# Optimization experiments

Measured on AMD Instinct MI355X. Metric: run time of the kernel, lower is better.

## Reference

```python
import jax, jax.numpy as jnp
import numpy as np

# Emformer config (from torchaudio.models.Emformer in BasicNet4)
D, H, FFN, L = 512, 4, 128, 4      # input_dim, num_heads, ffn_dim, num_layers
SEG, RC = 4, 1                     # segment_length, right_context_length
B, T = 8, 1025
U = T - RC                         # utterance length = 1024
NSEG = -(-U // SEG)                # 256 segments
R = NSEG * RC                      # total right-context frames = 256
DH = D // H


def _right_context_indices():
    # torchaudio _gen_right_context: segment i's right context = frames [(i+1)*SEG : (i+1)*SEG+RC],
    # last block = input[T-RC:]
    idx = [np.arange((i + 1) * SEG, (i + 1) * SEG + RC) for i in range(NSEG - 1)]
    idx.append(np.arange(T - RC, T))
    return np.concatenate(idx)


def _attention_mask():
    # Rows / cols ordered [right-context blocks (seg order), utterance frames].
    # A query belonging to segment i may attend to segment i's right-context block
    # and segment i's utterance frames (left_context_length=0, no memory bank).
    seg_rc = np.repeat(np.arange(NSEG), RC)
    seg_u = np.arange(U) // SEG
    seg_q = np.concatenate([seg_rc, seg_u])
    seg_k = np.concatenate([seg_rc, seg_u])
    return seg_q[:, None] == seg_k[None, :]  # (R+U, R+U), True = allowed


def _ln(x, g, b, eps=1e-5):
    mu = jnp.mean(x, -1, keepdims=True)
    var = jnp.mean(jnp.square(x - mu), -1, keepdims=True)
    return (x - mu) * jax.lax.rsqrt(var + eps) * g + b


def setup_inputs() -> dict:
    key = jax.random.key(0)
    ks = jax.random.split(key, 8)
    s = 0.02
    return {
        "x": jax.random.normal(ks[0], (B, T, D), jnp.float32),
        "Wq": jax.random.normal(ks[1], (L, D, D), jnp.float32) * s,
        "bq": jnp.zeros((L, D), jnp.float32),
        "Wkv": jax.random.normal(ks[2], (L, 2 * D, D), jnp.float32) * s,
        "bkv": jnp.zeros((L, 2 * D), jnp.float32),
        "Wo": jax.random.normal(ks[3], (L, D, D), jnp.float32) * s,
        "bo": jnp.zeros((L, D), jnp.float32),
        "W1": jax.random.normal(ks[4], (L, FFN, D), jnp.float32) * s,
        "b1": jnp.zeros((L, FFN), jnp.float32),
        "W2": jax.random.normal(ks[5], (L, D, FFN), jnp.float32) * s,
        "b2": jnp.zeros((L, D), jnp.float32),
        "ln_in_g": jnp.ones((L, D), jnp.float32),
        "ln_in_b": jnp.zeros((L, D), jnp.float32),
        "ff_ln_g": jnp.ones((L, D), jnp.float32),
        "ff_ln_b": jnp.zeros((L, D), jnp.float32),
        "ln_out_g": jnp.ones((L, D), jnp.float32),
        "ln_out_b": jnp.zeros((L, D), jnp.float32),
    }


def reference(x, Wq, bq, Wkv, bkv, Wo, bo, W1, b1, W2, b2,
              ln_in_g, ln_in_b, ff_ln_g, ff_ln_b, ln_out_g, ln_out_b):
    rc_idx = jnp.asarray(_right_context_indices())
    allowed = jnp.asarray(_attention_mask())
    scale = DH ** -0.5
    u = x[:, :U]          # (B, U, D) utterance
    r = x[:, rc_idx]      # (B, R, D) gathered right-context blocks
    for l in range(L):
        cat = jnp.concatenate([r, u], axis=1)            # (B, R+U, D)
        ln = _ln(cat, ln_in_g[l], ln_in_b[l])            # pre-attention LN
        q = (ln @ Wq[l].T + bq[l]).reshape(B, R + U, H, DH)
        kv = ln @ Wkv[l].T + bkv[l]
        k = kv[..., :D].reshape(B, R + U, H, DH)
        v = kv[..., D:].reshape(B, R + U, H, DH)
        scores = jnp.einsum("bqhd,bkhd->bhqk", q * scale, k)
        scores = jnp.where(allowed, scores, -jnp.inf)
        probs = jax.nn.softmax(scores, axis=-1)
        attn = jnp.einsum("bhqk,bkhd->bqhd", probs, v).reshape(B, R + U, D)
        rc_out = attn @ Wo[l].T + bo[l] + cat            # residual w/ pre-LN input
        h = _ln(rc_out, ff_ln_g[l], ff_ln_b[l])
        h = jax.nn.relu(h @ W1[l].T + b1[l]) @ W2[l].T + b2[l]
        rc_out = _ln(rc_out + h, ln_out_g[l], ln_out_b[l])
        r, u = rc_out[:, :R], rc_out[:, R:]
    return u.mean(axis=1)  # (B, D): mean-pool over utterance frames
```

## Files before the change

kernel.cpp:

```cpp
#include <hip/hip_runtime.h>
#include <cstdint>
#include <cstddef>

#define D_    512
#define H_    4
#define DH_   128
#define FFN_  128
#define L_    4
#define B_    8
#define T_    1025
#define U_    1024
#define NSEG_ 256
#define R_    256
#define TOT_  1280
#define M_    (B_*TOT_)
#define CH_   1536

typedef __attribute__((ext_vector_type(8))) short bf16x8;
typedef __attribute__((ext_vector_type(4))) float f32x4;
typedef unsigned short u16;

__device__ __forceinline__ u16 f2bf(float f) {
  unsigned u = __builtin_bit_cast(unsigned, f);
  u += 0x7fff + ((u >> 16) & 1);
  return (u16)(u >> 16);
}
__device__ __forceinline__ float bf2f(u16 h) {
  unsigned u = ((unsigned)h) << 16;
  return __builtin_bit_cast(float, u);
}

__device__ __forceinline__ void gload_lds16(const void* g, void* l) {
  __builtin_amdgcn_global_load_lds(
      (const __attribute__((address_space(1))) unsigned*)g,
      (__attribute__((address_space(3))) unsigned*)l, 16, 0, 0);
}

__global__ __launch_bounds__(256)
void cvt_all_k(const float* __restrict__ Wq, const float* __restrict__ Wkv,
               const float* __restrict__ Wo, const float* __restrict__ W1,
               const float* __restrict__ W2, const float* __restrict__ bq,
               const float* __restrict__ bkv,
               u16* __restrict__ WQKVb, u16* __restrict__ Wob,
               u16* __restrict__ W1b, u16* __restrict__ W2b,
               float* __restrict__ bQKV) {
  int i4 = blockIdx.x * 256 + threadIdx.x;
  if (i4 < 786432) {
    int e = i4 * 4;
    int l = e / 786432;
    int rem = e - l * 786432;
    int n = rem >> 9, k = rem & 511;
    const float* src = (n < 512) ? (Wq + (size_t)l * 262144 + n * 512 + k)
                                 : (Wkv + (size_t)l * 524288 + (n - 512) * 512 + k);
    float4 v = *(const float4*)src;
    ushort4 o; o.x = f2bf(v.x); o.y = f2bf(v.y); o.z = f2bf(v.z); o.w = f2bf(v.w);
    *(ushort4*)(WQKVb + e) = o;
  } else if (i4 < 1048576) {
    int e = (i4 - 786432) * 4;
    float4 v = *(const float4*)(Wo + e);
    ushort4 o; o.x = f2bf(v.x); o.y = f2bf(v.y); o.z = f2bf(v.z); o.w = f2bf(v.w);
    *(ushort4*)(Wob + e) = o;
  } else if (i4 < 1114112) {
    int e = (i4 - 1048576) * 4;
    float4 v = *(const float4*)(W1 + e);
    ushort4 o; o.x = f2bf(v.x); o.y = f2bf(v.y); o.z = f2bf(v.z); o.w = f2bf(v.w);
    *(ushort4*)(W1b + e) = o;
  } else if (i4 < 1179648) {
    int e = (i4 - 1114112) * 4;
    float4 v = *(const float4*)(W2 + e);
    ushort4 o; o.x = f2bf(v.x); o.y = f2bf(v.y); o.z = f2bf(v.z); o.w = f2bf(v.w);
    *(ushort4*)(W2b + e) = o;
  } else if (i4 < 1181184) {
    int e = (i4 - 1179648) * 4;
    int l = e / 1536, n = e - l * 1536;
#pragma unroll
    for (int t = 0; t < 4; ++t) {
      int nn = n + t;
      bQKV[e + t] = (nn < 512) ? bq[l * 512 + nn] : bkv[l * 1024 + (nn - 512)];
    }
  }
}

__global__ __launch_bounds__(256)
void gather_ln_k(const float* __restrict__ x, const float* __restrict__ g,
                 const float* __restrict__ bb, float* __restrict__ X,
                 u16* __restrict__ LNb) {
  int row = blockIdx.x;
  int tid = threadIdx.x;
  int b = row / TOT_, p = row % TOT_;
  int t = (p < R_) ? ((p < R_ - 1) ? 4 * (p + 1) : (T_ - 1)) : (p - R_);
  const float* xr = x + ((size_t)b * T_ + t) * D_;
  float e0 = xr[tid], e1 = xr[tid + 256];
  X[(size_t)row * D_ + tid] = e0;
  X[(size_t)row * D_ + tid + 256] = e1;
  float s = e0 + e1, ss = e0 * e0 + e1 * e1;
#pragma unroll
  for (int off = 32; off > 0; off >>= 1) {
    s  += __shfl_down(s, off);
    ss += __shfl_down(ss, off);
  }
  __shared__ float red[10];
  int wid = tid >> 6, lane = tid & 63;
  if (lane == 0) { red[wid] = s; red[4 + wid] = ss; }
  __syncthreads();
  if (tid == 0) {
    float S = red[0] + red[1] + red[2] + red[3];
    float SS = red[4] + red[5] + red[6] + red[7];
    float mu = S * (1.0f / D_);
    float var = SS * (1.0f / D_) - mu * mu;
    if (var < 0.f) var = 0.f;
    red[8] = mu; red[9] = rsqrtf(var + 1e-5f);
  }
  __syncthreads();
  float mu = red[8], rs = red[9];
  u16* yr = LNb + (size_t)row * D_;
  yr[tid]       = f2bf((e0 - mu) * rs * g[tid]       + bb[tid]);
  yr[tid + 256] = f2bf((e1 - mu) * rs * g[tid + 256] + bb[tid + 256]);
}

#define GBM 128
#define GBN 128
#define GBK 32

__global__ __launch_bounds__(256)
void gemm_qkv(const u16* __restrict__ A, const u16* __restrict__ Bw,
              const float* __restrict__ bias, u16* __restrict__ Cout,
              int M, int N, int K) {
  __shared__ __align__(16) u16 As[GBM * GBK];
  __shared__ __align__(16) u16 Bs[GBN * GBK];
  const int tid = threadIdx.x;
  const int wid = tid >> 6;
  const int lane = tid & 63;
  const int bm = blockIdx.y * GBM;
  const int bn = blockIdx.x * GBN;
  const int wr = wid >> 1, wc = wid & 1;

  const int srow = tid >> 2;
  const int skoff = (tid & 3) << 3;

  f32x4 acc[4][4] = {};

  const u16* Ag0 = A  + (size_t)(bm + srow)      * K + skoff;
  const u16* Ag1 = A  + (size_t)(bm + 64 + srow) * K + skoff;
  const u16* Bg0 = Bw + (size_t)(bn + srow)      * K + skoff;
  const u16* Bg1 = Bw + (size_t)(bn + 64 + srow) * K + skoff;
  u16* AsW0 = &As[(size_t)(wid * 16)      * GBK];
  u16* AsW1 = &As[(size_t)(64 + wid * 16) * GBK];
  u16* BsW0 = &Bs[(size_t)(wid * 16)      * GBK];
  u16* BsW1 = &Bs[(size_t)(64 + wid * 16) * GBK];

  const int lrow = lane & 15;
  const int lko  = (lane >> 4) * 16;

  for (int k0 = 0; k0 < K; k0 += GBK) {
    __syncthreads();
    gload_lds16(Ag0 + k0, AsW0);
    gload_lds16(Ag1 + k0, AsW1);
    gload_lds16(Bg0 + k0, BsW0);
    gload_lds16(Bg1 + k0, BsW1);
    __syncthreads();

    bf16x8 afrag[4], bfrag[4];
#pragma unroll
    for (int m = 0; m < 4; ++m) {
      int row = wr * 64 + m * 16 + lrow;
      afrag[m] = *(const bf16x8*)((const char*)As + row * (GBK * 2) + lko);
    }
#pragma unroll
    for (int n = 0; n < 4; ++n) {
      int col = wc * 64 + n * 16 + lrow;
      bfrag[n] = *(const bf16x8*)((const char*)Bs + col * (GBK * 2) + lko);
    }
#pragma unroll
    for (int m = 0; m < 4; ++m)
#pragma unroll
      for (int n = 0; n < 4; ++n)
        acc[m][n] = __builtin_amdgcn_mfma_f32_16x16x32_bf16(
            afrag[m], bfrag[n], acc[m][n], 0, 0, 0);
  }

  const int lcol  = lane & 15;
  const int lrow4 = (lane >> 4) * 4;
#pragma unroll
  for (int m = 0; m < 4; ++m) {
    int rowbase = bm + wr * 64 + m * 16 + lrow4;
#pragma unroll
    for (int n = 0; n < 4; ++n) {
      int col = bn + wc * 64 + n * 16 + lcol;
      float bv = bias[col];
#pragma unroll
      for (int j = 0; j < 4; ++j) {
        int row = rowbase + j;
        ((u16*)Cout)[(size_t)row * N + col] = f2bf(acc[m][n][j] + bv);
      }
    }
  }
}

template <int MODE>
__global__ __launch_bounds__(256)
void gemm_row_ln(const u16* __restrict__ A, const u16* __restrict__ Bw,
                 const float* __restrict__ bias, const float* __restrict__ Rsd,
                 float* __restrict__ Xout,
                 const float* __restrict__ g1, const float* __restrict__ b1,
                 const float* __restrict__ g2, const float* __restrict__ b2,
                 u16* __restrict__ OutBf, int K) {
  __shared__ __align__(16) u16 As[32 * 32];
  __shared__ __align__(16) u16 Bs[512 * 32];
  __shared__ float wsum[4][32], wss[4][32], mu_s[32], rs_s[32];
  const int tid = threadIdx.x;
  const int wid = tid >> 6, lane = tid & 63;
  const int bm = blockIdx.x * 32;
  const int l4 = lane >> 2;
  const int k8 = (lane & 3) << 3;
  const int lrow = lane & 15;
  const int lko  = (lane >> 4) * 16;

  f32x4 acc[2][8] = {};

  const u16* Ag = A + (size_t)(bm + (wid & 1) * 16 + l4) * K + k8;

  for (int k0 = 0; k0 < K; k0 += 32) {
    __syncthreads();
    if (wid < 2)
      gload_lds16(Ag + k0, (char*)As + (wid * 16) * 64);
#pragma unroll
    for (int p = 0; p < 8; ++p) {
      int row = wid * 128 + p * 16 + l4;
      gload_lds16(Bw + (size_t)row * K + k0 + k8,
                  (char*)Bs + (wid * 128 + p * 16) * 64);
    }
    __syncthreads();

    bf16x8 af[2], bf[8];
#pragma unroll
    for (int m = 0; m < 2; ++m)
      af[m] = *(const bf16x8*)((const char*)As + (m * 16 + lrow) * 64 + lko);
#pragma unroll
    for (int n = 0; n < 8; ++n)
      bf[n] = *(const bf16x8*)((const char*)Bs + (wid * 128 + n * 16 + lrow) * 64 + lko);
#pragma unroll
    for (int m = 0; m < 2; ++m)
#pragma unroll
      for (int n = 0; n < 8; ++n)
        acc[m][n] = __builtin_amdgcn_mfma_f32_16x16x32_bf16(
            af[m], bf[n], acc[m][n], 0, 0, 0);
  }

  const int lcol = lane & 15;
  const int lr4 = (lane >> 4) * 4;
#pragma unroll
  for (int n = 0; n < 8; ++n) {
    int col = wid * 128 + n * 16 + lcol;
    float bv = bias[col];
#pragma unroll
    for (int m = 0; m < 2; ++m)
#pragma unroll
      for (int j = 0; j < 4; ++j) {
        int row = bm + m * 16 + lr4 + j;
        float t = acc[m][n][j] + bv + Rsd[(size_t)row * D_ + col];
        if (MODE == 0) Xout[(size_t)row * D_ + col] = t;
        acc[m][n][j] = t;
      }
  }

  {
    float s0[2][4] = {}, s1[2][4] = {};
#pragma unroll
    for (int m = 0; m < 2; ++m)
#pragma unroll
      for (int n = 0; n < 8; ++n)
#pragma unroll
        for (int j = 0; j < 4; ++j) {
          float v = acc[m][n][j];
          s0[m][j] += v; s1[m][j] += v * v;
        }
#pragma unroll
    for (int off = 1; off < 16; off <<= 1)
#pragma unroll
      for (int m = 0; m < 2; ++m)
#pragma unroll
        for (int j = 0; j < 4; ++j) {
          s0[m][j] += __shfl_xor(s0[m][j], off);
          s1[m][j] += __shfl_xor(s1[m][j], off);
        }
    if ((lane & 15) == 0) {
#pragma unroll
      for (int m = 0; m < 2; ++m)
#pragma unroll
        for (int j = 0; j < 4; ++j) {
          int r = m * 16 + lr4 + j;
          wsum[wid][r] = s0[m][j]; wss[wid][r] = s1[m][j];
        }
    }
  }
  __syncthreads();
  if (tid < 32) {
    float S  = wsum[0][tid] + wsum[1][tid] + wsum[2][tid] + wsum[3][tid];
    float SS = wss[0][tid] + wss[1][tid] + wss[2][tid] + wss[3][tid];
    float mu = S * (1.0f / D_);
    float var = SS * (1.0f / D_) - mu * mu;
    if (var < 0.f) var = 0.f;
    mu_s[tid] = mu; rs_s[tid] = rsqrtf(var + 1e-5f);
  }
  __syncthreads();

  float gg[8], bv2[8];
#pragma unroll
  for (int n = 0; n < 8; ++n) {
    int col = wid * 128 + n * 16 + lcol;
    gg[n] = g1[col]; bv2[n] = b1[col];
  }
#pragma unroll
  for (int m = 0; m < 2; ++m)
#pragma unroll
    for (int n = 0; n < 8; ++n) {
      int col = wid * 128 + n * 16 + lcol;
#pragma unroll
      for (int j = 0; j < 4; ++j) {
        int r = m * 16 + lr4 + j;
        int row = bm + r;
        float ln = (acc[m][n][j] - mu_s[r]) * rs_s[r] * gg[n] + bv2[n];
        if (MODE == 0) {
          OutBf[(size_t)row * D_ + col] = f2bf(ln);
        } else {
          Xout[(size_t)row * D_ + col] = ln;
          acc[m][n][j] = ln;
        }
      }
    }

  if (MODE == 1) {
    __syncthreads();
    {
      float s0[2][4] = {}, s1[2][4] = {};
#pragma unroll
      for (int m = 0; m < 2; ++m)
#pragma unroll
        for (int n = 0; n < 8; ++n)
#pragma unroll
          for (int j = 0; j < 4; ++j) {
            float v = acc[m][n][j];
            s0[m][j] += v; s1[m][j] += v * v;
          }
#pragma unroll
      for (int off = 1; off < 16; off <<= 1)
#pragma unroll
        for (int m = 0; m < 2; ++m)
#pragma unroll
          for (int j = 0; j < 4; ++j) {
            s0[m][j] += __shfl_xor(s0[m][j], off);
            s1[m][j] += __shfl_xor(s1[m][j], off);
          }
      if ((lane & 15) == 0) {
#pragma unroll
        for (int m = 0; m < 2; ++m)
#pragma unroll
          for (int j = 0; j < 4; ++j) {
            int r = m * 16 + lr4 + j;
            wsum[wid][r] = s0[m][j]; wss[wid][r] = s1[m][j];
          }
      }
    }
    __syncthreads();
    if (tid < 32) {
      float S  = wsum[0][tid] + wsum[1][tid] + wsum[2][tid] + wsum[3][tid];
      float SS = wss[0][tid] + wss[1][tid] + wss[2][tid] + wss[3][tid];
      float mu = S * (1.0f / D_);
      float var = SS * (1.0f / D_) - mu * mu;
      if (var < 0.f) var = 0.f;
      mu_s[tid] = mu; rs_s[tid] = rsqrtf(var + 1e-5f);
    }
    __syncthreads();
#pragma unroll
    for (int n = 0; n < 8; ++n) {
      int col = wid * 128 + n * 16 + lcol;
      gg[n] = g2[col]; bv2[n] = b2[col];
    }
#pragma unroll
    for (int m = 0; m < 2; ++m)
#pragma unroll
      for (int n = 0; n < 8; ++n) {
        int col = wid * 128 + n * 16 + lcol;
#pragma unroll
        for (int j = 0; j < 4; ++j) {
          int r = m * 16 + lr4 + j;
          int row = bm + r;
          float ln = (acc[m][n][j] - mu_s[r]) * rs_s[r] * gg[n] + bv2[n];
          OutBf[(size_t)row * D_ + col] = f2bf(ln);
        }
      }
  }
}

__global__ __launch_bounds__(256)
void gemm_ffn1(const u16* __restrict__ A, const u16* __restrict__ Bw,
               const float* __restrict__ bias, u16* __restrict__ Hout) {
  __shared__ __align__(16) u16 As[32 * 32];
  __shared__ __align__(16) u16 Bs[128 * 32];
  const int tid = threadIdx.x;
  const int wid = tid >> 6, lane = tid & 63;
  const int bm = blockIdx.x * 32;
  const int l4 = lane >> 2;
  const int k8 = (lane & 3) << 3;
  const int lrow = lane & 15;
  const int lko  = (lane >> 4) * 16;

  f32x4 acc[2][2] = {};
  const u16* Ag = A + (size_t)(bm + (wid & 1) * 16 + l4) * D_ + k8;

  for (int k0 = 0; k0 < D_; k0 += 32) {
    __syncthreads();
    if (wid < 2)
      gload_lds16(Ag + k0, (char*)As + (wid * 16) * 64);
#pragma unroll
    for (int p = 0; p < 2; ++p) {
      int row = wid * 32 + p * 16 + l4;
      gload_lds16(Bw + (size_t)row * D_ + k0 + k8,
                  (char*)Bs + (wid * 32 + p * 16) * 64);
    }
    __syncthreads();
    bf16x8 af[2], bf[2];
#pragma unroll
    for (int m = 0; m < 2; ++m)
      af[m] = *(const bf16x8*)((const char*)As + (m * 16 + lrow) * 64 + lko);
#pragma unroll
    for (int n = 0; n < 2; ++n)
      bf[n] = *(const bf16x8*)((const char*)Bs + (wid * 32 + n * 16 + lrow) * 64 + lko);
#pragma unroll
    for (int m = 0; m < 2; ++m)
#pragma unroll
      for (int n = 0; n < 2; ++n)
        acc[m][n] = __builtin_amdgcn_mfma_f32_16x16x32_bf16(
            af[m], bf[n], acc[m][n], 0, 0, 0);
  }

  const int lcol = lane & 15;
  const int lr4 = (lane >> 4) * 4;
#pragma unroll
  for (int m = 0; m < 2; ++m)
#pragma unroll
    for (int n = 0; n < 2; ++n) {
      int col = wid * 32 + n * 16 + lcol;
      float bv = bias[col];
#pragma unroll
      for (int j = 0; j < 4; ++j) {
        int row = bm + m * 16 + lr4 + j;
        float v = fmaxf(acc[m][n][j] + bv, 0.f);
        Hout[(size_t)row * FFN_ + col] = f2bf(v);
      }
    }
}

#define QLD 516
__global__ __launch_bounds__(256)
void attn_k(const u16* __restrict__ QKV, u16* __restrict__ O) {
  int bs = blockIdx.x;
  int b = bs >> 8, s = bs & 255;
  __shared__ float Qs[5][QLD];
  __shared__ float Ks[5][QLD];
  __shared__ float Vs[5][QLD];
  __shared__ float P[H_][5][5];
  int tid = threadIdx.x;
  const float scale = 0.08838834764831845f;
  int rows[5];
  rows[0] = s;
#pragma unroll
  for (int i = 1; i < 5; ++i) rows[i] = R_ + 4 * s + (i - 1);
  for (int idx = tid; idx < 5 * D_; idx += 256) {
    int i = idx >> 9, c = idx & (D_ - 1);
    size_t base = ((size_t)b * TOT_ + rows[i]) * CH_;
    Qs[i][c] = bf2f(QKV[base + c]) * scale;
    Ks[i][c] = bf2f(QKV[base + D_ + c]);
    Vs[i][c] = bf2f(QKV[base + 2 * D_ + c]);
  }
  __syncthreads();
  int h = tid >> 6, lane = tid & 63;
  if (lane < 25) {
    int i = lane / 5, j = lane % 5;
    float sum = 0.f;
    const float* qp = &Qs[i][h * DH_];
    const float* kp = &Ks[j][h * DH_];
#pragma unroll 8
    for (int d = 0; d < DH_; ++d) sum += qp[d] * kp[d];
    P[h][i][j] = sum;
  }
  __syncthreads();
  if (lane < 5) {
    int i = lane;
    float m = P[h][i][0];
#pragma unroll
    for (int j = 1; j < 5; ++j) m = fmaxf(m, P[h][i][j]);
    float e[5], ssum = 0.f;
#pragma unroll
    for (int j = 0; j < 5; ++j) { e[j] = __expf(P[h][i][j] - m); ssum += e[j]; }
    float inv = 1.0f / ssum;
#pragma unroll
    for (int j = 0; j < 5; ++j) P[h][i][j] = e[j] * inv;
  }
  __syncthreads();
  for (int idx = lane; idx < 5 * DH_; idx += 64) {
    int i = idx >> 7, d = idx & (DH_ - 1);
    float o = 0.f;
#pragma unroll
    for (int j = 0; j < 5; ++j) o += P[h][i][j] * Vs[j][h * DH_ + d];
    O[((size_t)b * TOT_ + rows[i]) * D_ + h * DH_ + d] = f2bf(o);
  }
}

__global__ __launch_bounds__(256)
void mean_part_k(const float* __restrict__ X, float* __restrict__ part) {
  int d = blockIdx.x * 256 + threadIdx.x;
  int jc = blockIdx.y;
  int b = blockIdx.z;
  float acc = 0.f;
  const float* base = X + ((size_t)b * TOT_ + R_ + jc * 128) * D_ + d;
  for (int j = 0; j < 128; ++j) acc += base[(size_t)j * D_];
  part[((size_t)b * 8 + jc) * D_ + d] = acc;
}

__global__ __launch_bounds__(256)
void mean_final_k(const float* __restrict__ part, float* __restrict__ out) {
  int i = blockIdx.x * 256 + threadIdx.x;
  int b = i >> 9, d = i & (D_ - 1);
  float acc = 0.f;
#pragma unroll
  for (int c = 0; c < 8; ++c) acc += part[((size_t)b * 8 + c) * D_ + d];
  out[i] = acc * (1.0f / U_);
}

extern "C" void kernel_launch(void* const* d_in, const int* in_sizes, int n_in,
                              void* d_out, int out_size, void* d_ws, size_t ws_size,
                              hipStream_t stream) {
  const float* x      = (const float*)d_in[0];
  const float* Wq     = (const float*)d_in[1];
  const float* bq     = (const float*)d_in[2];
  const float* Wkv    = (const float*)d_in[3];
  const float* bkv    = (const float*)d_in[4];
  const float* Wo     = (const float*)d_in[5];
  const float* bo     = (const float*)d_in[6];
  const float* W1     = (const float*)d_in[7];
  const float* b1     = (const float*)d_in[8];
  const float* W2     = (const float*)d_in[9];
  const float* b2     = (const float*)d_in[10];
  const float* ln_in_g  = (const float*)d_in[11];
  const float* ln_in_b  = (const float*)d_in[12];
  const float* ff_ln_g  = (const float*)d_in[13];
  const float* ff_ln_b  = (const float*)d_in[14];
  const float* ln_out_g = (const float*)d_in[15];
  const float* ln_out_b = (const float*)d_in[16];
  float* out = (float*)d_out;

  char* wsb = (char*)d_ws;
  float* X     = (float*)wsb;
  u16*   LNbuf = (u16*)(wsb + 20971520);
  u16*   QKV   = (u16*)(wsb + 31457280);
  u16*   ATT   = (u16*)(wsb + 62914560);
  u16*   LN2b  = (u16*)(wsb + 73400320);
  u16*   Hb    = (u16*)(wsb + 83886080);
  float* part  = (float*)(wsb + 86507520);
  u16*   WQKVb = (u16*)(wsb + 86638592);
  u16*   Wob   = (u16*)(wsb + 92930048);
  u16*   W1b   = (u16*)(wsb + 95027200);
  u16*   W2b   = (u16*)(wsb + 95551488);
  float* bQKV  = (float*)(wsb + 96075776);

  cvt_all_k<<<4614, 256, 0, stream>>>(Wq, Wkv, Wo, W1, W2, bq, bkv,
                                      WQKVb, Wob, W1b, W2b, bQKV);
  gather_ln_k<<<M_, 256, 0, stream>>>(x, ln_in_g, ln_in_b, X, LNbuf);

  for (int l = 0; l < L_; ++l) {
    const u16* WQKV_l = WQKVb + (size_t)l * CH_ * D_;
    const u16* Wo_l   = Wob   + (size_t)l * D_ * D_;
    const u16* W1_l   = W1b   + (size_t)l * FFN_ * D_;
    const u16* W2_l   = W2b   + (size_t)l * D_ * FFN_;
    const float* bQKV_l = bQKV + (size_t)l * CH_;
    const float* bo_l = bo + (size_t)l * D_;
    const float* b1_l = b1 + (size_t)l * FFN_;
    const float* b2_l = b2 + (size_t)l * D_;

    gemm_qkv<<<dim3(CH_ / GBN, M_ / GBM), 256, 0, stream>>>(
        LNbuf, WQKV_l, bQKV_l, QKV, M_, CH_, D_);

    attn_k<<<B_ * NSEG_, 256, 0, stream>>>(QKV, ATT);

    gemm_row_ln<0><<<M_ / 32, 256, 0, stream>>>(
        ATT, Wo_l, bo_l, X, X,
        ff_ln_g + l * D_, ff_ln_b + l * D_, nullptr, nullptr, LN2b, D_);

    gemm_ffn1<<<M_ / 32, 256, 0, stream>>>(LN2b, W1_l, b1_l, Hb);

    if (l < L_ - 1) {
      gemm_row_ln<1><<<M_ / 32, 256, 0, stream>>>(
          Hb, W2_l, b2_l, X, X,
          ln_out_g + l * D_, ln_out_b + l * D_,
          ln_in_g + (l + 1) * D_, ln_in_b + (l + 1) * D_, LNbuf, FFN_);
    } else {
      gemm_row_ln<2><<<M_ / 32, 256, 0, stream>>>(
          Hb, W2_l, b2_l, X, X,
          ln_out_g + l * D_, ln_out_b + l * D_,
          nullptr, nullptr, nullptr, FFN_);
    }
  }

  mean_part_k<<<dim3(2, 8, 8), 256, 0, stream>>>(X, part);
  mean_final_k<<<(B_ * D_) / 256, 256, 0, stream>>>(part, out);
}
```

Baseline: 437.7 us.

## Halve row tiles in LN GEMMs, swizzle QKV grid per XCD, vectorize attention loads

```diff
diff --git a/kernel.cpp b/kernel.cpp
--- a/kernel.cpp
+++ b/kernel.cpp
@@ -118,21 +118,23 @@
   yr[tid + 256] = f2bf((e1 - mu) * rs * g[tid + 256] + bb[tid + 256]);
 }
 
-#define GBM 128
-#define GBN 128
 #define GBK 32
 
 __global__ __launch_bounds__(256)
 void gemm_qkv(const u16* __restrict__ A, const u16* __restrict__ Bw,
-              const float* __restrict__ bias, u16* __restrict__ Cout,
-              int M, int N, int K) {
-  __shared__ __align__(16) u16 As[GBM * GBK];
-  __shared__ __align__(16) u16 Bs[GBN * GBK];
+              const float* __restrict__ bias, u16* __restrict__ Cout) {
+  __shared__ __align__(16) u16 As[128 * GBK];
+  __shared__ __align__(16) u16 Bs[128 * GBK];
   const int tid = threadIdx.x;
   const int wid = tid >> 6;
   const int lane = tid & 63;
-  const int bm = blockIdx.y * GBM;
-  const int bn = blockIdx.x * GBN;
+  const int bid = blockIdx.x;
+  const int xcd = bid & 7;
+  const int t = bid >> 3;
+  const int cb = t % 12;
+  const int rb = xcd * 10 + t / 12;
+  const int bm = rb * 128;
+  const int bn = cb * 128;
   const int wr = wid >> 1, wc = wid & 1;
 
   const int srow = tid >> 2;
@@ -140,10 +142,10 @@
 
   f32x4 acc[4][4] = {};
 
-  const u16* Ag0 = A  + (size_t)(bm + srow)      * K + skoff;
-  const u16* Ag1 = A  + (size_t)(bm + 64 + srow) * K + skoff;
-  const u16* Bg0 = Bw + (size_t)(bn + srow)      * K + skoff;
-  const u16* Bg1 = Bw + (size_t)(bn + 64 + srow) * K + skoff;
+  const u16* Ag0 = A  + (size_t)(bm + srow)      * D_ + skoff;
+  const u16* Ag1 = A  + (size_t)(bm + 64 + srow) * D_ + skoff;
+  const u16* Bg0 = Bw + (size_t)(bn + srow)      * D_ + skoff;
+  const u16* Bg1 = Bw + (size_t)(bn + 64 + srow) * D_ + skoff;
   u16* AsW0 = &As[(size_t)(wid * 16)      * GBK];
   u16* AsW1 = &As[(size_t)(64 + wid * 16) * GBK];
   u16* BsW0 = &Bs[(size_t)(wid * 16)      * GBK];
@@ -152,7 +154,7 @@
   const int lrow = lane & 15;
   const int lko  = (lane >> 4) * 16;
 
-  for (int k0 = 0; k0 < K; k0 += GBK) {
+  for (int k0 = 0; k0 < D_; k0 += GBK) {
     __syncthreads();
     gload_lds16(Ag0 + k0, AsW0);
     gload_lds16(Ag1 + k0, AsW1);
@@ -191,7 +193,7 @@
 #pragma unroll
       for (int j = 0; j < 4; ++j) {
         int row = rowbase + j;
-        ((u16*)Cout)[(size_t)row * N + col] = f2bf(acc[m][n][j] + bv);
+        Cout[(size_t)row * CH_ + col] = f2bf(acc[m][n][j] + bv);
       }
     }
   }
@@ -205,25 +207,25 @@
                  const float* __restrict__ g1, const float* __restrict__ b1,
                  const float* __restrict__ g2, const float* __restrict__ b2,
                  u16* __restrict__ OutBf, int K) {
-  __shared__ __align__(16) u16 As[32 * 32];
+  __shared__ __align__(16) u16 As[16 * 32];
   __shared__ __align__(16) u16 Bs[512 * 32];
-  __shared__ float wsum[4][32], wss[4][32], mu_s[32], rs_s[32];
+  __shared__ float wsum[4][16], wss[4][16], mu_s[16], rs_s[16];
   const int tid = threadIdx.x;
   const int wid = tid >> 6, lane = tid & 63;
-  const int bm = blockIdx.x * 32;
+  const int bm = blockIdx.x * 16;
   const int l4 = lane >> 2;
   const int k8 = (lane & 3) << 3;
   const int lrow = lane & 15;
   const int lko  = (lane >> 4) * 16;
 
-  f32x4 acc[2][8] = {};
-
-  const u16* Ag = A + (size_t)(bm + (wid & 1) * 16 + l4) * K + k8;
+  f32x4 acc[8] = {};
+
+  const u16* Ag = A + (size_t)(bm + l4) * K + k8;
 
   for (int k0 = 0; k0 < K; k0 += 32) {
     __syncthreads();
-    if (wid < 2)
-      gload_lds16(Ag + k0, (char*)As + (wid * 16) * 64);
+    if (wid == 0)
+      gload_lds16(Ag + k0, As);
 #pragma unroll
     for (int p = 0; p < 8; ++p) {
       int row = wid * 128 + p * 16 + l4;
@@ -232,19 +234,14 @@
     }
     __syncthreads();
 
-    bf16x8 af[2], bf[8];
-#pragma unroll
-    for (int m = 0; m < 2; ++m)
-      af[m] = *(const bf16x8*)((const char*)As + (m * 16 + lrow) * 64 + lko);
+    bf16x8 af = *(const bf16x8*)((const char*)As + lrow * 64 + lko);
+    bf16x8 bf[8];
 #pragma unroll
     for (int n = 0; n < 8; ++n)
       bf[n] = *(const bf16x8*)((const char*)Bs + (wid * 128 + n * 16 + lrow) * 64 + lko);
 #pragma unroll
-    for (int m = 0; m < 2; ++m)
-#pragma unroll
-      for (int n = 0; n < 8; ++n)
-        acc[m][n] = __builtin_amdgcn_mfma_f32_16x16x32_bf16(
-            af[m], bf[n], acc[m][n], 0, 0, 0);
+    for (int n = 0; n < 8; ++n)
+      acc[n] = __builtin_amdgcn_mfma_f32_16x16x32_bf16(af, bf[n], acc[n], 0, 0, 0);
   }
 
   const int lcol = lane & 15;
@@ -254,48 +251,39 @@
     int col = wid * 128 + n * 16 + lcol;
     float bv = bias[col];
 #pragma unroll
-    for (int m = 0; m < 2; ++m)
+    for (int j = 0; j < 4; ++j) {
+      int row = bm + lr4 + j;
+      float t = acc[n][j] + bv + Rsd[(size_t)row * D_ + col];
+      if (MODE == 0) Xout[(size_t)row * D_ + col] = t;
+      acc[n][j] = t;
+    }
+  }
+
+  {
+    float s0[4] = {}, s1[4] = {};
+#pragma unroll
+    for (int n = 0; n < 8; ++n)
 #pragma unroll
       for (int j = 0; j < 4; ++j) {
-        int row = bm + m * 16 + lr4 + j;
-        float t = acc[m][n][j] + bv + Rsd[(size_t)row * D_ + col];
-        if (MODE == 0) Xout[(size_t)row * D_ + col] = t;
-        acc[m][n][j] = t;
-      }
-  }
-
-  {
-    float s0[2][4] = {}, s1[2][4] = {};
-#pragma unroll
-    for (int m = 0; m < 2; ++m)
-#pragma unroll
-      for (int n = 0; n < 8; ++n)
-#pragma unroll
-        for (int j = 0; j < 4; ++j) {
-          float v = acc[m][n][j];
-          s0[m][j] += v; s1[m][j] += v * v;
-        }
+        float v = acc[n][j];
+        s0[j] += v; s1[j] += v * v;
+      }
 #pragma unroll
     for (int off = 1; off < 16; off <<= 1)
 #pragma unroll
-      for (int m = 0; m < 2; ++m)
-#pragma unroll
-        for (int j = 0; j < 4; ++j) {
-          s0[m][j] += __shfl_xor(s0[m][j], off);
-          s1[m][j] += __shfl_xor(s1[m][j], off);
-        }
+      for (int j = 0; j < 4; ++j) {
+        s0[j] += __shfl_xor(s0[j], off);
+        s1[j] += __shfl_xor(s1[j], off);
+      }
     if ((lane & 15) == 0) {
 #pragma unroll
-      for (int m = 0; m < 2; ++m)
-#pragma unroll
-        for (int j = 0; j < 4; ++j) {
-          int r = m * 16 + lr4 + j;
-          wsum[wid][r] = s0[m][j]; wss[wid][r] = s1[m][j];
-        }
-    }
-  }
-  __syncthreads();
-  if (tid < 32) {
+      for (int j = 0; j < 4; ++j) {
+        wsum[wid][lr4 + j] = s0[j]; wss[wid][lr4 + j] = s1[j];
+      }
+    }
+  }
+  __syncthreads();
+  if (tid < 16) {
     float S  = wsum[0][tid] + wsum[1][tid] + wsum[2][tid] + wsum[3][tid];
     float SS = wss[0][tid] + wss[1][tid] + wss[2][tid] + wss[3][tid];
     float mu = S * (1.0f / D_);
@@ -312,58 +300,49 @@
     gg[n] = g1[col]; bv2[n] = b1[col];
   }
 #pragma unroll
-  for (int m = 0; m < 2; ++m)
-#pragma unroll
-    for (int n = 0; n < 8; ++n) {
-      int col = wid * 128 + n * 16 + lcol;
-#pragma unroll
-      for (int j = 0; j < 4; ++j) {
-        int r = m * 16 + lr4 + j;
-        int row = bm + r;
-        float ln = (acc[m][n][j] - mu_s[r]) * rs_s[r] * gg[n] + bv2[n];
-        if (MODE == 0) {
-          OutBf[(size_t)row * D_ + col] = f2bf(ln);
-        } else {
-          Xout[(size_t)row * D_ + col] = ln;
-          acc[m][n][j] = ln;
+  for (int n = 0; n < 8; ++n) {
+    int col = wid * 128 + n * 16 + lcol;
+#pragma unroll
+    for (int j = 0; j < 4; ++j) {
+      int r = lr4 + j;
+      int row = bm + r;
+      float ln = (acc[n][j] - mu_s[r]) * rs_s[r] * gg[n] + bv2[n];
+      if (MODE == 0) {
+        OutBf[(size_t)row * D_ + col] = f2bf(ln);
+      } else {
+        Xout[(size_t)row * D_ + col] = ln;
+        acc[n][j] = ln;
+      }
+    }
+  }
+
+  if (MODE == 1) {
+    __syncthreads();
+    {
+      float s0[4] = {}, s1[4] = {};
+#pragma unroll
+      for (int n = 0; n < 8; ++n)
+#pragma unroll
+        for (int j = 0; j < 4; ++j) {
+          float v = acc[n][j];
+          s0[j] += v; s1[j] += v * v;
         }
-      }
-    }
-
-  if (MODE == 1) {
-    __syncthreads();
-    {
-      float s0[2][4] = {}, s1[2][4] = {};
-#pragma unroll
-      for (int m = 0; m < 2; ++m)
-#pragma unroll
-        for (int n = 0; n < 8; ++n)
-#pragma unroll
-          for (int j = 0; j < 4; ++j) {
-            float v = acc[m][n][j];
-            s0[m][j] += v; s1[m][j] += v * v;
-          }
 #pragma unroll
       for (int off = 1; off < 16; off <<= 1)
 #pragma unroll
-        for (int m = 0; m < 2; ++m)
-#pragma unroll
-          for (int j = 0; j < 4; ++j) {
-            s0[m][j] += __shfl_xor(s0[m][j], off);
-            s1[m][j] += __shfl_xor(s1[m][j], off);
-          }
+        for (int j = 0; j < 4; ++j) {
+          s0[j] += __shfl_xor(s0[j], off);
+          s1[j] += __shfl_xor(s1[j], off);
+        }
       if ((lane & 15) == 0) {
 #pragma unroll
-        for (int m = 0; m < 2; ++m)
-#pragma unroll
-          for (int j = 0; j < 4; ++j) {
-            int r = m * 16 + lr4 + j;
-            wsum[wid][r] = s0[m][j]; wss[wid][r] = s1[m][j];
-          }
-      }
-    }
-    __syncthreads();
-    if (tid < 32) {
+        for (int j = 0; j < 4; ++j) {
+          wsum[wid][lr4 + j] = s0[j]; wss[wid][lr4 + j] = s1[j];
+        }
+      }
+    }
+    __syncthreads();
+    if (tid < 16) {
       float S  = wsum[0][tid] + wsum[1][tid] + wsum[2][tid] + wsum[3][tid];
       float SS = wss[0][tid] + wss[1][tid] + wss[2][tid] + wss[3][tid];
       float mu = S * (1.0f / D_);
@@ -378,41 +357,39 @@
       gg[n] = g2[col]; bv2[n] = b2[col];
     }
 #pragma unroll
-    for (int m = 0; m < 2; ++m)
-#pragma unroll
-      for (int n = 0; n < 8; ++n) {
-        int col = wid * 128 + n * 16 + lcol;
-#pragma unroll
-        for (int j = 0; j < 4; ++j) {
-          int r = m * 16 + lr4 + j;
-          int row = bm + r;
-          float ln = (acc[m][n][j] - mu_s[r]) * rs_s[r] * gg[n] + bv2[n];
-          OutBf[(size_t)row * D_ + col] = f2bf(ln);
-        }
-      }
+    for (int n = 0; n < 8; ++n) {
+      int col = wid * 128 + n * 16 + lcol;
+#pragma unroll
+      for (int j = 0; j < 4; ++j) {
+        int r = lr4 + j;
+        int row = bm + r;
+        float ln = (acc[n][j] - mu_s[r]) * rs_s[r] * gg[n] + bv2[n];
+        OutBf[(size_t)row * D_ + col] = f2bf(ln);
+      }
+    }
   }
 }
 
 __global__ __launch_bounds__(256)
 void gemm_ffn1(const u16* __restrict__ A, const u16* __restrict__ Bw,
                const float* __restrict__ bias, u16* __restrict__ Hout) {
-  __shared__ __align__(16) u16 As[32 * 32];
+  __shared__ __align__(16) u16 As[16 * 32];
   __shared__ __align__(16) u16 Bs[128 * 32];
   const int tid = threadIdx.x;
   const int wid = tid >> 6, lane = tid & 63;
-  const int bm = blockIdx.x * 32;
+  const int bm = blockIdx.x * 16;
   const int l4 = lane >> 2;
   const int k8 = (lane & 3) << 3;
   const int lrow = lane & 15;
   const int lko  = (lane >> 4) * 16;
 
-  f32x4 acc[2][2] = {};
-  const u16* Ag = A + (size_t)(bm + (wid & 1) * 16 + l4) * D_ + k8;
+  f32x4 acc[2] = {};
+  const u16* Ag = A + (size_t)(bm + l4) * D_ + k8;
 
   for (int k0 = 0; k0 < D_; k0 += 32) {
     __syncthreads();
-    if (wid < 2)
-      gload_lds16(Ag + k0, (char*)As + (wid * 16) * 64);
+    if (wid == 0)
+      gload_lds16(Ag + k0, As);
 #pragma unroll
     for (int p = 0; p < 2; ++p) {
       int row = wid * 32 + p * 16 + l4;
@@ -420,36 +397,29 @@
                   (char*)Bs + (wid * 32 + p * 16) * 64);
     }
     __syncthreads();
-    bf16x8 af[2], bf[2];
-#pragma unroll
-    for (int m = 0; m < 2; ++m)
-      af[m] = *(const bf16x8*)((const char*)As + (m * 16 + lrow) * 64 + lko);
+    bf16x8 af = *(const bf16x8*)((const char*)As + lrow * 64 + lko);
+    bf16x8 bf[2];
 #pragma unroll
     for (int n = 0; n < 2; ++n)
       bf[n] = *(const bf16x8*)((const char*)Bs + (wid * 32 + n * 16 + lrow) * 64 + lko);
 #pragma unroll
-    for (int m = 0; m < 2; ++m)
-#pragma unroll
-      for (int n = 0; n < 2; ++n)
-        acc[m][n] = __builtin_amdgcn_mfma_f32_16x16x32_bf16(
-            af[m], bf[n], acc[m][n], 0, 0, 0);
+    for (int n = 0; n < 2; ++n)
+      acc[n] = __builtin_amdgcn_mfma_f32_16x16x32_bf16(af, bf[n], acc[n], 0, 0, 0);
   }
 
   const int lcol = lane & 15;
   const int lr4 = (lane >> 4) * 4;
 #pragma unroll
-  for (int m = 0; m < 2; ++m)
-#pragma unroll
-    for (int n = 0; n < 2; ++n) {
-      int col = wid * 32 + n * 16 + lcol;
-      float bv = bias[col];
-#pragma unroll
-      for (int j = 0; j < 4; ++j) {
-        int row = bm + m * 16 + lr4 + j;
-        float v = fmaxf(acc[m][n][j] + bv, 0.f);
-        Hout[(size_t)row * FFN_ + col] = f2bf(v);
-      }
-    }
+  for (int n = 0; n < 2; ++n) {
+    int col = wid * 32 + n * 16 + lcol;
+    float bv = bias[col];
+#pragma unroll
+    for (int j = 0; j < 4; ++j) {
+      int row = bm + lr4 + j;
+      float v = fmaxf(acc[n][j] + bv, 0.f);
+      Hout[(size_t)row * FFN_ + col] = f2bf(v);
+    }
+  }
 }
 
 #define QLD 516
@@ -467,12 +437,20 @@
   rows[0] = s;
 #pragma unroll
   for (int i = 1; i < 5; ++i) rows[i] = R_ + 4 * s + (i - 1);
-  for (int idx = tid; idx < 5 * D_; idx += 256) {
-    int i = idx >> 9, c = idx & (D_ - 1);
-    size_t base = ((size_t)b * TOT_ + rows[i]) * CH_;
-    Qs[i][c] = bf2f(QKV[base + c]) * scale;
-    Ks[i][c] = bf2f(QKV[base + D_ + c]);
-    Vs[i][c] = bf2f(QKV[base + 2 * D_ + c]);
+  for (int idx = tid; idx < 960; idx += 256) {
+    int mtx = idx / 320;
+    int rem = idx - mtx * 320;
+    int i = rem >> 6, c8 = rem & 63;
+    size_t base = ((size_t)b * TOT_ + rows[i]) * CH_ + mtx * 512 + c8 * 8;
+    bf16x8 v = *(const bf16x8*)(QKV + base);
+    float* dst = (mtx == 0) ? &Qs[i][c8 * 8] : (mtx == 1 ? &Ks[i][c8 * 8] : &Vs[i][c8 * 8]);
+    if (mtx == 0) {
+#pragma unroll
+      for (int t = 0; t < 8; ++t) dst[t] = bf2f((u16)v[t]) * scale;
+    } else {
+#pragma unroll
+      for (int t = 0; t < 8; ++t) dst[t] = bf2f((u16)v[t]);
+    }
   }
   __syncthreads();
   int h = tid >> 6, lane = tid & 63;
@@ -579,24 +557,23 @@
     const float* b1_l = b1 + (size_t)l * FFN_;
     const float* b2_l = b2 + (size_t)l * D_;
 
-    gemm_qkv<<<dim3(CH_ / GBN, M_ / GBM), 256, 0, stream>>>(
-        LNbuf, WQKV_l, bQKV_l, QKV, M_, CH_, D_);
+    gemm_qkv<<<960, 256, 0, stream>>>(LNbuf, WQKV_l, bQKV_l, QKV);
 
     attn_k<<<B_ * NSEG_, 256, 0, stream>>>(QKV, ATT);
 
-    gemm_row_ln<0><<<M_ / 32, 256, 0, stream>>>(
+    gemm_row_ln<0><<<M_ / 16, 256, 0, stream>>>(
         ATT, Wo_l, bo_l, X, X,
         ff_ln_g + l * D_, ff_ln_b + l * D_, nullptr, nullptr, LN2b, D_);
 
-    gemm_ffn1<<<M_ / 32, 256, 0, stream>>>(LN2b, W1_l, b1_l, Hb);
+    gemm_ffn1<<<M_ / 16, 256, 0, stream>>>(LN2b, W1_l, b1_l, Hb);
 
     if (l < L_ - 1) {
-      gemm_row_ln<1><<<M_ / 32, 256, 0, stream>>>(
+      gemm_row_ln<1><<<M_ / 16, 256, 0, stream>>>(
           Hb, W2_l, b2_l, X, X,
           ln_out_g + l * D_, ln_out_b + l * D_,
           ln_in_g + (l + 1) * D_, ln_in_b + (l + 1) * D_, LNbuf, FFN_);
     } else {
-      gemm_row_ln<2><<<M_ / 32, 256, 0, stream>>>(
+      gemm_row_ln<2><<<M_ / 16, 256, 0, stream>>>(
           Hb, W2_l, b2_l, X, X,
           ln_out_g + l * D_, ln_out_b + l * D_,
           nullptr, nullptr, nullptr, FFN_);
```

New measurement: 438.6 us. About the same (+0.2%).
